# Optimization experiments

Measured on AMD Instinct MI355X. Metric: run time of the kernel, lower is better.

## Reference

```python
import jax, jax.numpy as jnp
import numpy as np

MARGIN_1 = 0.3
ALPHA_1 = 0.5
EPS = 1e-12
NEG = -1e30


def setup_inputs() -> dict:
    key = jax.random.key(0)
    batch_size = 128
    d = 2048
    N = 2 * batch_size
    feature = jax.random.normal(key, (N, d), dtype=jnp.float32)
    # PK-sampled ids: 32 identities x 4 instances, same ids in both modality halves
    num_ids = 32
    ids = jnp.repeat(jnp.arange(num_ids, dtype=jnp.int32), batch_size // num_ids)
    targets = jnp.concatenate([ids, ids])  # (N,)
    return {"feature": feature, "targets": targets}


def reference(feature, targets):
    N = feature.shape[0]
    # modality indicator: first half 0, second half 1 (self.sub)
    sub = jnp.arange(N) >= (N // 2)
    G = feature @ feature.T  # (N, N) gram matrix, symmetric

    pos_mat = targets[:, None] == targets[None, :]   # is_pos per anchor row
    intra_mat = sub[:, None] == sub[None, :]          # intra-modality per anchor row

    def msm(col_mask):
        # row-wise softmax of G restricted to columns in col_mask, zeros elsewhere
        logits = jnp.where(col_mask[None, :], G, NEG)
        return jax.nn.softmax(logits, axis=-1) * col_mask[None, :].astype(G.dtype)

    def trans(row_mask, col_mask):
        # ab: (intra rows -> cross cols) transition probs; ba: (cross -> intra)
        ab = msm(col_mask)
        ba = msm(row_mask)  # G symmetric, so softmax over row_mask cols == match.T softmax
        t = ab @ ba  # round-trip transition probability, valid on row_mask x row_mask
        return jnp.sqrt(jnp.clip(t, EPS))

    def masked_mean(v, m):
        mf = m.astype(v.dtype)
        w = mf[:, None] * mf[None, :]
        return jnp.sum(v * w) / jnp.sum(w)

    def per_anchor(is_pos, intra):
        is_neg = ~is_pos
        cross = ~intra
        mpi = is_pos & intra
        mpc = is_pos & cross
        mni = is_neg & intra
        mnc = is_neg & cross
        t_pos = trans(mpi, mpc)
        t_neg = trans(mni, mnc)
        loss_ap = masked_mean(jnp.clip(t_neg + (MARGIN_1 - ALPHA_1), 0.0, None), mni)
        loss_an = masked_mean(jnp.clip(ALPHA_1 - t_pos, 0.0, None), mpi)
        return loss_ap + loss_an

    loss = jnp.mean(jax.vmap(per_anchor)(pos_mat, intra_mat))

    # hard-mining accuracy over euclidean distance matrix
    sq = jnp.sum(feature * feature, axis=1)
    dist = jnp.sqrt(jnp.clip(sq[:, None] + sq[None, :] - 2.0 * G, EPS))
    dist_ap = jnp.max(jnp.where(pos_mat, dist, -jnp.inf), axis=1)
    dist_an = jnp.min(jnp.where(~pos_mat, dist, jnp.inf), axis=1)
    correct = jnp.sum((dist_an >= dist_ap).astype(jnp.int32))
    return loss, correct
```

## Files before the change

kernel.cpp:

```cpp
#include <hip/hip_runtime.h>

#define EPSF 1e-12f

typedef short bf16x8 __attribute__((ext_vector_type(8)));
typedef float f32x4 __attribute__((ext_vector_type(4)));

__device__ __forceinline__ unsigned short f2bf(float f) {
  unsigned int u = __float_as_uint(f);
  unsigned int r = u + 0x7fffu + ((u >> 16) & 1u);
  return (unsigned short)(r >> 16);
}

__global__ void gemm_tile(const float* __restrict__ F, float* __restrict__ Gout,
                          int n, int d, int kchunk) {
  __shared__ float As[64][36];
  __shared__ float Bs[64][36];
  const int tid = threadIdx.x;
  const int bx = blockIdx.x, by = blockIdx.y, kz = blockIdx.z;
  const int ty = tid >> 4, tx = tid & 15;
  const int lrow = tid >> 2;
  const int lcol = (tid & 3) * 8;
  const float* Ap = F + (size_t)(bx * 64 + lrow) * d + (size_t)kz * kchunk + lcol;
  const float* Bp = F + (size_t)(by * 64 + lrow) * d + (size_t)kz * kchunk + lcol;
  float acc[4][4];
  for (int r = 0; r < 4; r++)
    for (int c = 0; c < 4; c++) acc[r][c] = 0.0f;

  for (int ks = 0; ks < kchunk; ks += 32) {
    float4 a0 = *(const float4*)(Ap + ks);
    float4 a1 = *(const float4*)(Ap + ks + 4);
    float4 b0 = *(const float4*)(Bp + ks);
    float4 b1 = *(const float4*)(Bp + ks + 4);
    __syncthreads();
    *(float4*)&As[lrow][lcol]     = a0;
    *(float4*)&As[lrow][lcol + 4] = a1;
    *(float4*)&Bs[lrow][lcol]     = b0;
    *(float4*)&Bs[lrow][lcol + 4] = b1;
    __syncthreads();
#pragma unroll
    for (int kk = 0; kk < 32; kk += 4) {
      float4 av[4], bv[4];
#pragma unroll
      for (int r = 0; r < 4; r++) av[r] = *(const float4*)&As[ty + 16 * r][kk];
#pragma unroll
      for (int c = 0; c < 4; c++) bv[c] = *(const float4*)&Bs[tx + 16 * c][kk];
#pragma unroll
      for (int r = 0; r < 4; r++) {
        float4 A = av[r];
#pragma unroll
        for (int c = 0; c < 4; c++) {
          float4 B = bv[c];
          acc[r][c] += A.x * B.x + A.y * B.y + A.z * B.z + A.w * B.w;
        }
      }
    }
  }
  float* Gs = Gout + (size_t)kz * n * n;
#pragma unroll
  for (int r = 0; r < 4; r++)
#pragma unroll
    for (int c = 0; c < 4; c++)
      Gs[(size_t)(bx * 64 + ty + 16 * r) * n + (by * 64 + tx + 16 * c)] =
          acc[r][c];
}

__global__ void stats_kernel(const float* __restrict__ Gp,
                             const int* __restrict__ targets,
                             float* __restrict__ G, float* __restrict__ LSEtab,
                             float* __restrict__ flags, int n, int S) {
  __shared__ float bins[4][33];
  __shared__ int tg[256];
  __shared__ float diag[256];
  const int tid = threadIdx.x;
  const int lane = tid & 63;
  const int w = tid >> 6;
  const int nn = n * n;
  tg[tid] = targets[tid];
  {
    float s0 = 0.0f;
    for (int s = 0; s < S; s++)
      s0 += Gp[(size_t)s * nn + (size_t)tid * (n + 1)];
    diag[tid] = s0;
  }
  if (tid < 128) bins[tid >> 5][tid & 31] = 0.0f;
  __syncthreads();

  const int r = blockIdx.x * 4 + w;
  const int nhalf = n >> 1;
  const int opp0 = (r < nhalf) ? nhalf : 0;
  const int myid = tg[r];
  const float sqr = diag[r];

  float4 v = make_float4(0.f, 0.f, 0.f, 0.f);
  for (int s = 0; s < S; s++) {
    float4 t = *(const float4*)(Gp + (size_t)s * nn + (size_t)r * n + lane * 4);
    v.x += t.x; v.y += t.y; v.z += t.z; v.w += t.w;
  }
  *(float4*)(G + (size_t)r * n + lane * 4) = v;
  float gv[4] = {v.x, v.y, v.z, v.w};

  float dap = -1e30f, dan = 1e30f;
#pragma unroll
  for (int q = 0; q < 4; q++) {
    int j = lane * 4 + q;
    float dist = sqrtf(fmaxf(sqr + diag[j] - 2.0f * gv[q], EPSF));
    if (tg[j] == myid) dap = fmaxf(dap, dist);
    else               dan = fminf(dan, dist);
  }
#pragma unroll
  for (int off = 32; off; off >>= 1) {
    dap = fmaxf(dap, __shfl_xor(dap, off));
    dan = fminf(dan, __shfl_xor(dan, off));
  }
  if (lane == 0) flags[r] = (dan >= dap) ? 1.0f : 0.0f;

  float mx = -1e30f;
#pragma unroll
  for (int q = 0; q < 4; q++) {
    int j = lane * 4 + q;
    if (j >= opp0 && j < opp0 + nhalf) mx = fmaxf(mx, gv[q]);
  }
#pragma unroll
  for (int off = 32; off; off >>= 1) mx = fmaxf(mx, __shfl_xor(mx, off));

#pragma unroll
  for (int q = 0; q < 4; q++) {
    int j = lane * 4 + q;
    if (j >= opp0 && j < opp0 + nhalf)
      atomicAdd(&bins[w][tg[j]], __expf(gv[q] - mx));
  }
  __syncthreads();

  if (lane < 32) {
    float b = bins[w][lane];
    float lv = __shfl_up(b, 1, 32);
    if (lane == 0) lv = 0.0f;
#pragma unroll
    for (int off = 1; off < 32; off <<= 1) {
      float t = __shfl_up(lv, off, 32);
      if (lane >= off) lv += t;
    }
    float rv = __shfl_down(b, 1, 32);
    if (lane == 31) rv = 0.0f;
#pragma unroll
    for (int off = 1; off < 32; off <<= 1) {
      float t = __shfl_down(rv, off, 32);
      if (lane + off < 32) rv += t;
    }
    float excl = fmaxf(lv + rv, 1e-37f);
    LSEtab[(size_t)lane * n + r] = mx + __logf(excl);
  }
}

__global__ void TransitionLoss_30666066494151_kernel(
    const float* __restrict__ G, const int* __restrict__ targets,
    const float* __restrict__ LSEtab, float* __restrict__ lsp,
    float* __restrict__ lan, float* __restrict__ cnts, int n) {
  __shared__ unsigned short W[128][136];
  __shared__ int tg[256];
  __shared__ int maskA[128], maskB[128];
  __shared__ float Ri[128], Cl[128];
  __shared__ float SMRAW[16][17], SP[16][17], SQ[16][17];
  __shared__ float red[256];
  __shared__ int Plist[16], Qlist[16];
  __shared__ int ctrP, ctrQ;

  const int tid = threadIdx.x;
  const int cls = blockIdx.x;
  const int nhalf = n >> 1;
  const int myid = cls & 31;
  const int hA = cls >> 5;
  const int rowA0 = hA * nhalf;
  const int colB0 = nhalf - rowA0;

  tg[tid] = targets[tid];
  if (tid == 0) { ctrP = 0; ctrQ = 0; }
  __syncthreads();

  if (tid < 128) {
    maskA[tid] = (tg[rowA0 + tid] != myid) ? 1 : 0;
    Ri[tid] = LSEtab[(size_t)myid * n + rowA0 + tid];
  } else {
    maskB[tid - 128] = (tg[colB0 + tid - 128] != myid) ? 1 : 0;
    Cl[tid - 128] = LSEtab[(size_t)myid * n + colB0 + tid - 128];
  }
  if (tg[tid] == myid) {
    int inAhalf = (((tid >= nhalf) ? 1 : 0) == hA) ? 1 : 0;
    if (inAhalf) { int k = atomicAdd(&ctrP, 1); if (k < 16) Plist[k] = tid; }
    else         { int k = atomicAdd(&ctrQ, 1); if (k < 16) Qlist[k] = tid; }
  }
  __syncthreads();
  const int nP = min(ctrP, 16), nQ = min(ctrQ, 16);

#pragma unroll
  for (int k8 = 0; k8 < 2; k8++) {
    float4 g[8];
#pragma unroll
    for (int u = 0; u < 8; u++) {
      int e4 = tid + 256 * (k8 * 8 + u);
      int i = e4 >> 5;
      int l4 = (e4 & 31) << 2;
      g[u] = *(const float4*)(G + (size_t)(rowA0 + i) * n + colB0 + l4);
    }
#pragma unroll
    for (int u = 0; u < 8; u++) {
      int e4 = tid + 256 * (k8 * 8 + u);
      int i = e4 >> 5;
      int l4 = (e4 & 31) << 2;
      float rih = 0.5f * Ri[i];
      int ma = maskA[i];
      float w0 = (ma && maskB[l4 + 0]) ? __expf(g[u].x - rih - 0.5f * Cl[l4 + 0]) : 0.0f;
      float w1 = (ma && maskB[l4 + 1]) ? __expf(g[u].y - rih - 0.5f * Cl[l4 + 1]) : 0.0f;
      float w2 = (ma && maskB[l4 + 2]) ? __expf(g[u].z - rih - 0.5f * Cl[l4 + 2]) : 0.0f;
      float w3 = (ma && maskB[l4 + 3]) ? __expf(g[u].w - rih - 0.5f * Cl[l4 + 3]) : 0.0f;
      uint2 packed;
      packed.x = (unsigned)f2bf(w0) | ((unsigned)f2bf(w1) << 16);
      packed.y = (unsigned)f2bf(w2) | ((unsigned)f2bf(w3) << 16);
      *(uint2*)&W[i][l4] = packed;
    }
  }

  {
    int p = tid >> 4, q = tid & 15;
    float v = 0.0f;
    if (p < nP && q < nQ) v = G[(size_t)Plist[p] * n + Qlist[q]];
    SMRAW[p][q] = v;
  }
  __syncthreads();

  const int lane = tid & 63;
  const int wv = tid >> 6;
  const int m16 = lane & 15;
  const int kh = lane >> 4;
  f32x4 acc[2][8];
#pragma unroll
  for (int r = 0; r < 2; r++)
#pragma unroll
    for (int c = 0; c < 8; c++) acc[r][c] = (f32x4){0.f, 0.f, 0.f, 0.f};

#pragma unroll
  for (int kc = 0; kc < 4; kc++) {
    const int koff = kc * 32 + kh * 8;
    bf16x8 bfrag[8];
#pragma unroll
    for (int c = 0; c < 8; c++)
      bfrag[c] = *(const bf16x8*)&W[c * 16 + m16][koff];
#pragma unroll
    for (int r = 0; r < 2; r++) {
      bf16x8 afrag = bfrag[wv * 2 + r];
#pragma unroll
      for (int c = 0; c < 8; c++)
        acc[r][c] = __builtin_amdgcn_mfma_f32_16x16x32_bf16(
            afrag, bfrag[c], acc[r][c], 0, 0, 0);
    }
  }

  float lsum = 0.0f;
#pragma unroll
  for (int r = 0; r < 2; r++)
#pragma unroll
    for (int c = 0; c < 8; c++) {
      f32x4 D = acc[r][c];
      int jcol = c * 16 + m16;
      float rj = Ri[jcol];
#pragma unroll
      for (int e = 0; e < 4; e++) {
        int irow = wv * 32 + r * 16 + kh * 4 + e;
        float t = __expf(0.5f * (rj - Ri[irow])) * D[e];
        lsum += fmaxf(sqrtf(fmaxf(t, EPSF)) - 0.2f, 0.0f);
      }
    }
  red[tid] = lsum;
  __syncthreads();
  for (int s2 = 128; s2 > 0; s2 >>= 1) {
    if (tid < s2) red[tid] += red[tid + s2];
    __syncthreads();
  }
  if (tid == 0) lsp[cls] = red[0];

  __syncthreads();
  red[tid] = (tid < 128) ? (float)maskA[tid] : 0.0f;
  __syncthreads();
  for (int s2 = 128; s2 > 0; s2 >>= 1) {
    if (tid < s2) red[tid] += red[tid + s2];
    __syncthreads();
  }
  if (tid == 0) { cnts[cls * 2 + 0] = red[0]; cnts[cls * 2 + 1] = (float)nP; }

  if (tid < nP) {
    float mx = -1e30f;
    for (int q = 0; q < nQ; q++) mx = fmaxf(mx, SMRAW[tid][q]);
    float s = 0.0f;
    for (int q = 0; q < nQ; q++) s += __expf(SMRAW[tid][q] - mx);
    for (int q = 0; q < nQ; q++) SP[tid][q] = __expf(SMRAW[tid][q] - mx) / s;
  }
  if (tid >= 64 && tid < 64 + nQ) {
    int q = tid - 64;
    float mx = -1e30f;
    for (int p = 0; p < nP; p++) mx = fmaxf(mx, SMRAW[p][q]);
    float s = 0.0f;
    for (int p = 0; p < nP; p++) s += __expf(SMRAW[p][q] - mx);
    for (int p = 0; p < nP; p++) SQ[q][p] = __expf(SMRAW[p][q] - mx) / s;
  }
  __syncthreads();
  float lv = 0.0f;
  if (tid < nP * nP) {
    int i = tid / nP, j = tid - i * nP;
    float t = 0.0f;
    for (int l = 0; l < nQ; l++) t += SP[i][l] * SQ[l][j];
    lv = fmaxf(0.5f - sqrtf(fmaxf(t, EPSF)), 0.0f);
  }
  red[tid] = lv;
  __syncthreads();
  for (int s2 = 128; s2 > 0; s2 >>= 1) {
    if (tid < s2) red[tid] += red[tid + s2];
    __syncthreads();
  }
  if (tid == 0) lan[cls] = red[0];
}

__global__ void final_reduce(const float* __restrict__ lsp,
                             const float* __restrict__ lan,
                             const float* __restrict__ cnts,
                             const float* __restrict__ flags,
                             float* __restrict__ out, int n) {
  __shared__ float rl[256], rf[256];
  const int tid = threadIdx.x;
  float lv = 0.0f;
  if (tid < 64) {
    float nA = cnts[tid * 2 + 0];
    float nP = cnts[tid * 2 + 1];
    if (nP > 0.5f && nA > 0.5f)
      lv = nP * (lsp[tid] / (nA * nA) + lan[tid] / (nP * nP));
  }
  rl[tid] = lv;
  rf[tid] = flags[tid];
  __syncthreads();
  for (int s2 = 128; s2 > 0; s2 >>= 1) {
    if (tid < s2) { rl[tid] += rl[tid + s2]; rf[tid] += rf[tid + s2]; }
    __syncthreads();
  }
  if (tid == 0) {
    out[0] = rl[0] / (float)n;
    out[1] = rf[0];
  }
}

extern "C" void kernel_launch(void* const* d_in, const int* in_sizes, int n_in,
                              void* d_out, int out_size, void* d_ws,
                              size_t ws_size, hipStream_t stream) {
  const float* feature = (const float*)d_in[0];
  const int* targets = (const int*)d_in[1];
  const int n = in_sizes[1];
  const int d = in_sizes[0] / n;
  const int nn = n * n;
  const size_t small = 64 + 64 + 128 + 256 + (size_t)n * 32;

  int S = 1;
  if (ws_size >= (small + nn + (size_t)16 * nn) * sizeof(float)) S = 16;
  else if (ws_size >= (small + nn + (size_t)4 * nn) * sizeof(float)) S = 4;

  float* ws = (float*)d_ws;
  float* lsp = ws;
  float* lan = lsp + 64;
  float* cnts = lan + 64;
  float* flags = cnts + 128;
  float* LSEtab = flags + 256;
  float* G = LSEtab + (size_t)n * 32;
  float* Gp = (S > 1) ? (G + nn) : G;
  float* out = (float*)d_out;

  dim3 gg(n / 64, n / 64, S);
  gemm_tile<<<gg, 256, 0, stream>>>(feature, Gp, n, d, d / S);

  stats_kernel<<<n / 4, 256, 0, stream>>>(Gp, targets, G, LSEtab, flags, n, S);

  TransitionLoss_30666066494151_kernel<<<64, 256, 0, stream>>>(
      G, targets, LSEtab, lsp, lan, cnts, n);

  final_reduce<<<1, 256, 0, stream>>>(lsp, lan, cnts, flags, out, n);
}
```

Baseline: 62.37 us.

## Fuse four kernels into one persistent kernel with global atomic barriers

Merges the split-K GEMM, stats, transition-loss and final-reduce kernels into a single 256-block launch, replacing kernel boundaries with atomic-counter grid barriers and a shared-memory union. The aim is to remove launch gaps between the four stages. It adds a memset of the counters, spin-wait barriers that rely on all blocks being co-resident, and hardcodes the GEMM grid to 4x4 tiles with 256 blocks, which assumes S=16 and n=256.

```diff
diff --git a/kernel.cpp b/kernel.cpp
--- a/kernel.cpp
+++ b/kernel.cpp
@@ -11,338 +11,369 @@
   return (unsigned short)(r >> 16);
 }
 
-__global__ void gemm_tile(const float* __restrict__ F, float* __restrict__ Gout,
-                          int n, int d, int kchunk) {
-  __shared__ float As[64][36];
-  __shared__ float Bs[64][36];
+union SMem {
+  struct { float As[64][36]; float Bs[64][36]; } g;
+  struct {
+    unsigned short W[128][136];
+    int tg[256];
+    int maskA[128], maskB[128];
+    float Ri[128], Cl[128];
+    float SMRAW[16][17], SP[16][17], SQ[16][17];
+    float red[256];
+    int Plist[16], Qlist[16];
+    int ctrP, ctrQ;
+  } c;
+  struct { float bins[4][33]; int tg[256]; float diag[256]; } s;
+  struct { float rl[256]; float rf[256]; } f;
+};
+
+__device__ __forceinline__ void garrive(unsigned* ctr, int tid) {
+  __syncthreads();
+  if (tid == 0) {
+    __threadfence();
+    atomicAdd(ctr, 1u);
+  }
+}
+__device__ __forceinline__ void gbarrier(unsigned* ctr, unsigned tgt, int tid) {
+  __syncthreads();
+  if (tid == 0) {
+    __threadfence();
+    atomicAdd(ctr, 1u);
+    while (atomicAdd(ctr, 0u) < tgt) __builtin_amdgcn_s_sleep(1);
+    __threadfence();
+  }
+  __syncthreads();
+}
+
+__global__ __launch_bounds__(256, 2) void TransitionLoss_30666066494151_kernel(
+    const float* __restrict__ F, const int* __restrict__ targets,
+    unsigned* __restrict__ ctr, float* __restrict__ lsp,
+    float* __restrict__ lan, float* __restrict__ cnts,
+    float* __restrict__ flags, float* __restrict__ LSEtab,
+    float* __restrict__ G, float* __restrict__ Gp,
+    float* __restrict__ out, int n, int d, int S) {
+  __shared__ SMem sm;
   const int tid = threadIdx.x;
-  const int bx = blockIdx.x, by = blockIdx.y, kz = blockIdx.z;
-  const int ty = tid >> 4, tx = tid & 15;
-  const int lrow = tid >> 2;
-  const int lcol = (tid & 3) * 8;
-  const float* Ap = F + (size_t)(bx * 64 + lrow) * d + (size_t)kz * kchunk + lcol;
-  const float* Bp = F + (size_t)(by * 64 + lrow) * d + (size_t)kz * kchunk + lcol;
-  float acc[4][4];
-  for (int r = 0; r < 4; r++)
-    for (int c = 0; c < 4; c++) acc[r][c] = 0.0f;
-
-  for (int ks = 0; ks < kchunk; ks += 32) {
-    float4 a0 = *(const float4*)(Ap + ks);
-    float4 a1 = *(const float4*)(Ap + ks + 4);
-    float4 b0 = *(const float4*)(Bp + ks);
-    float4 b1 = *(const float4*)(Bp + ks + 4);
-    __syncthreads();
-    *(float4*)&As[lrow][lcol]     = a0;
-    *(float4*)&As[lrow][lcol + 4] = a1;
-    *(float4*)&Bs[lrow][lcol]     = b0;
-    *(float4*)&Bs[lrow][lcol + 4] = b1;
-    __syncthreads();
-#pragma unroll
-    for (int kk = 0; kk < 32; kk += 4) {
-      float4 av[4], bv[4];
-#pragma unroll
-      for (int r = 0; r < 4; r++) av[r] = *(const float4*)&As[ty + 16 * r][kk];
-#pragma unroll
-      for (int c = 0; c < 4; c++) bv[c] = *(const float4*)&Bs[tx + 16 * c][kk];
-#pragma unroll
-      for (int r = 0; r < 4; r++) {
-        float4 A = av[r];
-#pragma unroll
-        for (int c = 0; c < 4; c++) {
-          float4 B = bv[c];
-          acc[r][c] += A.x * B.x + A.y * B.y + A.z * B.z + A.w * B.w;
+  const int b = blockIdx.x;
+  const int nn = n * n;
+  const int nhalf = n >> 1;
+
+  if (b < 16 * S) {
+    const int bx = b & 3, by = (b >> 2) & 3, kz = b >> 4;
+    const int kchunk = d / S;
+    const int ty = tid >> 4, tx = tid & 15;
+    const int lrow = tid >> 2;
+    const int lcol = (tid & 3) * 8;
+    const float* Ap = F + (size_t)(bx * 64 + lrow) * d + (size_t)kz * kchunk + lcol;
+    const float* Bp = F + (size_t)(by * 64 + lrow) * d + (size_t)kz * kchunk + lcol;
+    float acc[4][4];
+    for (int r = 0; r < 4; r++)
+      for (int c = 0; c < 4; c++) acc[r][c] = 0.0f;
+
+    for (int ks = 0; ks < kchunk; ks += 32) {
+      float4 a0 = *(const float4*)(Ap + ks);
+      float4 a1 = *(const float4*)(Ap + ks + 4);
+      float4 b0 = *(const float4*)(Bp + ks);
+      float4 b1 = *(const float4*)(Bp + ks + 4);
+      __syncthreads();
+      *(float4*)&sm.g.As[lrow][lcol]     = a0;
+      *(float4*)&sm.g.As[lrow][lcol + 4] = a1;
+      *(float4*)&sm.g.Bs[lrow][lcol]     = b0;
+      *(float4*)&sm.g.Bs[lrow][lcol + 4] = b1;
+      __syncthreads();
+#pragma unroll
+      for (int kk = 0; kk < 32; kk += 4) {
+        float4 av[4], bv[4];
+#pragma unroll
+        for (int r = 0; r < 4; r++)
+          av[r] = *(const float4*)&sm.g.As[ty + 16 * r][kk];
+#pragma unroll
+        for (int c = 0; c < 4; c++)
+          bv[c] = *(const float4*)&sm.g.Bs[tx + 16 * c][kk];
+#pragma unroll
+        for (int r = 0; r < 4; r++) {
+          float4 A = av[r];
+#pragma unroll
+          for (int c = 0; c < 4; c++) {
+            float4 B = bv[c];
+            acc[r][c] += A.x * B.x + A.y * B.y + A.z * B.z + A.w * B.w;
+          }
         }
       }
     }
-  }
-  float* Gs = Gout + (size_t)kz * n * n;
-#pragma unroll
-  for (int r = 0; r < 4; r++)
-#pragma unroll
-    for (int c = 0; c < 4; c++)
-      Gs[(size_t)(bx * 64 + ty + 16 * r) * n + (by * 64 + tx + 16 * c)] =
-          acc[r][c];
-}
-
-__global__ void stats_kernel(const float* __restrict__ Gp,
-                             const int* __restrict__ targets,
-                             float* __restrict__ G, float* __restrict__ LSEtab,
-                             float* __restrict__ flags, int n, int S) {
-  __shared__ float bins[4][33];
-  __shared__ int tg[256];
-  __shared__ float diag[256];
-  const int tid = threadIdx.x;
-  const int lane = tid & 63;
-  const int w = tid >> 6;
-  const int nn = n * n;
-  tg[tid] = targets[tid];
+    float* Gs = Gp + (size_t)kz * nn;
+#pragma unroll
+    for (int r = 0; r < 4; r++)
+#pragma unroll
+      for (int c = 0; c < 4; c++)
+        Gs[(size_t)(bx * 64 + ty + 16 * r) * n + (by * 64 + tx + 16 * c)] =
+            acc[r][c];
+  }
+
+  if (b >= 64) { garrive(&ctr[0], tid); return; }
+  gbarrier(&ctr[0], 256, tid);
+
   {
-    float s0 = 0.0f;
-    for (int s = 0; s < S; s++)
-      s0 += Gp[(size_t)s * nn + (size_t)tid * (n + 1)];
-    diag[tid] = s0;
-  }
-  if (tid < 128) bins[tid >> 5][tid & 31] = 0.0f;
-  __syncthreads();
-
-  const int r = blockIdx.x * 4 + w;
-  const int nhalf = n >> 1;
-  const int opp0 = (r < nhalf) ? nhalf : 0;
-  const int myid = tg[r];
-  const float sqr = diag[r];
-
-  float4 v = make_float4(0.f, 0.f, 0.f, 0.f);
-  for (int s = 0; s < S; s++) {
-    float4 t = *(const float4*)(Gp + (size_t)s * nn + (size_t)r * n + lane * 4);
-    v.x += t.x; v.y += t.y; v.z += t.z; v.w += t.w;
-  }
-  *(float4*)(G + (size_t)r * n + lane * 4) = v;
-  float gv[4] = {v.x, v.y, v.z, v.w};
-
-  float dap = -1e30f, dan = 1e30f;
-#pragma unroll
-  for (int q = 0; q < 4; q++) {
-    int j = lane * 4 + q;
-    float dist = sqrtf(fmaxf(sqr + diag[j] - 2.0f * gv[q], EPSF));
-    if (tg[j] == myid) dap = fmaxf(dap, dist);
-    else               dan = fminf(dan, dist);
-  }
-#pragma unroll
-  for (int off = 32; off; off >>= 1) {
-    dap = fmaxf(dap, __shfl_xor(dap, off));
-    dan = fminf(dan, __shfl_xor(dan, off));
-  }
-  if (lane == 0) flags[r] = (dan >= dap) ? 1.0f : 0.0f;
-
-  float mx = -1e30f;
-#pragma unroll
-  for (int q = 0; q < 4; q++) {
-    int j = lane * 4 + q;
-    if (j >= opp0 && j < opp0 + nhalf) mx = fmaxf(mx, gv[q]);
-  }
-#pragma unroll
-  for (int off = 32; off; off >>= 1) mx = fmaxf(mx, __shfl_xor(mx, off));
-
-#pragma unroll
-  for (int q = 0; q < 4; q++) {
-    int j = lane * 4 + q;
-    if (j >= opp0 && j < opp0 + nhalf)
-      atomicAdd(&bins[w][tg[j]], __expf(gv[q] - mx));
-  }
-  __syncthreads();
-
-  if (lane < 32) {
-    float b = bins[w][lane];
-    float lv = __shfl_up(b, 1, 32);
-    if (lane == 0) lv = 0.0f;
-#pragma unroll
-    for (int off = 1; off < 32; off <<= 1) {
-      float t = __shfl_up(lv, off, 32);
-      if (lane >= off) lv += t;
-    }
-    float rv = __shfl_down(b, 1, 32);
-    if (lane == 31) rv = 0.0f;
-#pragma unroll
-    for (int off = 1; off < 32; off <<= 1) {
-      float t = __shfl_down(rv, off, 32);
-      if (lane + off < 32) rv += t;
-    }
-    float excl = fmaxf(lv + rv, 1e-37f);
-    LSEtab[(size_t)lane * n + r] = mx + __logf(excl);
-  }
-}
-
-__global__ void TransitionLoss_30666066494151_kernel(
-    const float* __restrict__ G, const int* __restrict__ targets,
-    const float* __restrict__ LSEtab, float* __restrict__ lsp,
-    float* __restrict__ lan, float* __restrict__ cnts, int n) {
-  __shared__ unsigned short W[128][136];
-  __shared__ int tg[256];
-  __shared__ int maskA[128], maskB[128];
-  __shared__ float Ri[128], Cl[128];
-  __shared__ float SMRAW[16][17], SP[16][17], SQ[16][17];
-  __shared__ float red[256];
-  __shared__ int Plist[16], Qlist[16];
-  __shared__ int ctrP, ctrQ;
-
-  const int tid = threadIdx.x;
-  const int cls = blockIdx.x;
-  const int nhalf = n >> 1;
-  const int myid = cls & 31;
-  const int hA = cls >> 5;
-  const int rowA0 = hA * nhalf;
-  const int colB0 = nhalf - rowA0;
-
-  tg[tid] = targets[tid];
-  if (tid == 0) { ctrP = 0; ctrQ = 0; }
-  __syncthreads();
-
-  if (tid < 128) {
-    maskA[tid] = (tg[rowA0 + tid] != myid) ? 1 : 0;
-    Ri[tid] = LSEtab[(size_t)myid * n + rowA0 + tid];
-  } else {
-    maskB[tid - 128] = (tg[colB0 + tid - 128] != myid) ? 1 : 0;
-    Cl[tid - 128] = LSEtab[(size_t)myid * n + colB0 + tid - 128];
-  }
-  if (tg[tid] == myid) {
-    int inAhalf = (((tid >= nhalf) ? 1 : 0) == hA) ? 1 : 0;
-    if (inAhalf) { int k = atomicAdd(&ctrP, 1); if (k < 16) Plist[k] = tid; }
-    else         { int k = atomicAdd(&ctrQ, 1); if (k < 16) Qlist[k] = tid; }
-  }
-  __syncthreads();
-  const int nP = min(ctrP, 16), nQ = min(ctrQ, 16);
-
-#pragma unroll
-  for (int k8 = 0; k8 < 2; k8++) {
-    float4 g[8];
-#pragma unroll
-    for (int u = 0; u < 8; u++) {
-      int e4 = tid + 256 * (k8 * 8 + u);
-      int i = e4 >> 5;
-      int l4 = (e4 & 31) << 2;
-      g[u] = *(const float4*)(G + (size_t)(rowA0 + i) * n + colB0 + l4);
-    }
-#pragma unroll
-    for (int u = 0; u < 8; u++) {
-      int e4 = tid + 256 * (k8 * 8 + u);
-      int i = e4 >> 5;
-      int l4 = (e4 & 31) << 2;
-      float rih = 0.5f * Ri[i];
-      int ma = maskA[i];
-      float w0 = (ma && maskB[l4 + 0]) ? __expf(g[u].x - rih - 0.5f * Cl[l4 + 0]) : 0.0f;
-      float w1 = (ma && maskB[l4 + 1]) ? __expf(g[u].y - rih - 0.5f * Cl[l4 + 1]) : 0.0f;
-      float w2 = (ma && maskB[l4 + 2]) ? __expf(g[u].z - rih - 0.5f * Cl[l4 + 2]) : 0.0f;
-      float w3 = (ma && maskB[l4 + 3]) ? __expf(g[u].w - rih - 0.5f * Cl[l4 + 3]) : 0.0f;
-      uint2 packed;
-      packed.x = (unsigned)f2bf(w0) | ((unsigned)f2bf(w1) << 16);
-      packed.y = (unsigned)f2bf(w2) | ((unsigned)f2bf(w3) << 16);
-      *(uint2*)&W[i][l4] = packed;
-    }
-  }
+    const int lane = tid & 63;
+    const int w = tid >> 6;
+    sm.s.tg[tid] = targets[tid];
+    {
+      float s0 = 0.0f;
+      for (int s = 0; s < S; s++)
+        s0 += Gp[(size_t)s * nn + (size_t)tid * (n + 1)];
+      sm.s.diag[tid] = s0;
+    }
+    if (tid < 128) sm.s.bins[tid >> 5][tid & 31] = 0.0f;
+    __syncthreads();
+
+    const int r = b * 4 + w;
+    const int opp0 = (r < nhalf) ? nhalf : 0;
+    const int myid = sm.s.tg[r];
+    const float sqr = sm.s.diag[r];
+
+    float4 v = make_float4(0.f, 0.f, 0.f, 0.f);
+    for (int s = 0; s < S; s++) {
+      float4 t = *(const float4*)(Gp + (size_t)s * nn + (size_t)r * n + lane * 4);
+      v.x += t.x; v.y += t.y; v.z += t.z; v.w += t.w;
+    }
+    *(float4*)(G + (size_t)r * n + lane * 4) = v;
+    float gv[4] = {v.x, v.y, v.z, v.w};
+
+    float dap = -1e30f, dan = 1e30f;
+#pragma unroll
+    for (int q = 0; q < 4; q++) {
+      int j = lane * 4 + q;
+      float dist = sqrtf(fmaxf(sqr + sm.s.diag[j] - 2.0f * gv[q], EPSF));
+      if (sm.s.tg[j] == myid) dap = fmaxf(dap, dist);
+      else                    dan = fminf(dan, dist);
+    }
+#pragma unroll
+    for (int off = 32; off; off >>= 1) {
+      dap = fmaxf(dap, __shfl_xor(dap, off));
+      dan = fminf(dan, __shfl_xor(dan, off));
+    }
+    if (lane == 0) flags[r] = (dan >= dap) ? 1.0f : 0.0f;
+
+    float mx = -1e30f;
+#pragma unroll
+    for (int q = 0; q < 4; q++) {
+      int j = lane * 4 + q;
+      if (j >= opp0 && j < opp0 + nhalf) mx = fmaxf(mx, gv[q]);
+    }
+#pragma unroll
+    for (int off = 32; off; off >>= 1) mx = fmaxf(mx, __shfl_xor(mx, off));
+
+#pragma unroll
+    for (int q = 0; q < 4; q++) {
+      int j = lane * 4 + q;
+      if (j >= opp0 && j < opp0 + nhalf)
+        atomicAdd(&sm.s.bins[w][sm.s.tg[j]], __expf(gv[q] - mx));
+    }
+    __syncthreads();
+
+    if (lane < 32) {
+      float bb = sm.s.bins[w][lane];
+      float lv = __shfl_up(bb, 1, 32);
+      if (lane == 0) lv = 0.0f;
+#pragma unroll
+      for (int off = 1; off < 32; off <<= 1) {
+        float t = __shfl_up(lv, off, 32);
+        if (lane >= off) lv += t;
+      }
+      float rvv = __shfl_down(bb, 1, 32);
+      if (lane == 31) rvv = 0.0f;
+#pragma unroll
+      for (int off = 1; off < 32; off <<= 1) {
+        float t = __shfl_down(rvv, off, 32);
+        if (lane + off < 32) rvv += t;
+      }
+      float excl = fmaxf(lv + rvv, 1e-37f);
+      LSEtab[(size_t)lane * n + r] = mx + __logf(excl);
+    }
+  }
+
+  gbarrier(&ctr[1], 64, tid);
 
   {
-    int p = tid >> 4, q = tid & 15;
-    float v = 0.0f;
-    if (p < nP && q < nQ) v = G[(size_t)Plist[p] * n + Qlist[q]];
-    SMRAW[p][q] = v;
-  }
-  __syncthreads();
-
-  const int lane = tid & 63;
-  const int wv = tid >> 6;
-  const int m16 = lane & 15;
-  const int kh = lane >> 4;
-  f32x4 acc[2][8];
-#pragma unroll
-  for (int r = 0; r < 2; r++)
-#pragma unroll
-    for (int c = 0; c < 8; c++) acc[r][c] = (f32x4){0.f, 0.f, 0.f, 0.f};
-
-#pragma unroll
-  for (int kc = 0; kc < 4; kc++) {
-    const int koff = kc * 32 + kh * 8;
-    bf16x8 bfrag[8];
-#pragma unroll
-    for (int c = 0; c < 8; c++)
-      bfrag[c] = *(const bf16x8*)&W[c * 16 + m16][koff];
-#pragma unroll
-    for (int r = 0; r < 2; r++) {
-      bf16x8 afrag = bfrag[wv * 2 + r];
+    const int cls = b;
+    const int myid = cls & 31;
+    const int hA = cls >> 5;
+    const int rowA0 = hA * nhalf;
+    const int colB0 = nhalf - rowA0;
+
+    sm.c.tg[tid] = targets[tid];
+    if (tid == 0) { sm.c.ctrP = 0; sm.c.ctrQ = 0; }
+    __syncthreads();
+
+    if (tid < 128) {
+      sm.c.maskA[tid] = (sm.c.tg[rowA0 + tid] != myid) ? 1 : 0;
+      sm.c.Ri[tid] = LSEtab[(size_t)myid * n + rowA0 + tid];
+    } else {
+      sm.c.maskB[tid - 128] = (sm.c.tg[colB0 + tid - 128] != myid) ? 1 : 0;
+      sm.c.Cl[tid - 128] = LSEtab[(size_t)myid * n + colB0 + tid - 128];
+    }
+    if (sm.c.tg[tid] == myid) {
+      int inAhalf = (((tid >= nhalf) ? 1 : 0) == hA) ? 1 : 0;
+      if (inAhalf) { int k = atomicAdd(&sm.c.ctrP, 1); if (k < 16) sm.c.Plist[k] = tid; }
+      else         { int k = atomicAdd(&sm.c.ctrQ, 1); if (k < 16) sm.c.Qlist[k] = tid; }
+    }
+    __syncthreads();
+    const int nP = min(sm.c.ctrP, 16), nQ = min(sm.c.ctrQ, 16);
+
+#pragma unroll
+    for (int k8 = 0; k8 < 2; k8++) {
+      float4 g[8];
+#pragma unroll
+      for (int u = 0; u < 8; u++) {
+        int e4 = tid + 256 * (k8 * 8 + u);
+        int i = e4 >> 5;
+        int l4 = (e4 & 31) << 2;
+        g[u] = *(const float4*)(G + (size_t)(rowA0 + i) * n + colB0 + l4);
+      }
+#pragma unroll
+      for (int u = 0; u < 8; u++) {
+        int e4 = tid + 256 * (k8 * 8 + u);
+        int i = e4 >> 5;
+        int l4 = (e4 & 31) << 2;
+        float rih = 0.5f * sm.c.Ri[i];
+        int ma = sm.c.maskA[i];
+        float w0 = (ma && sm.c.maskB[l4 + 0]) ? __expf(g[u].x - rih - 0.5f * sm.c.Cl[l4 + 0]) : 0.0f;
+        float w1 = (ma && sm.c.maskB[l4 + 1]) ? __expf(g[u].y - rih - 0.5f * sm.c.Cl[l4 + 1]) : 0.0f;
+        float w2 = (ma && sm.c.maskB[l4 + 2]) ? __expf(g[u].z - rih - 0.5f * sm.c.Cl[l4 + 2]) : 0.0f;
+        float w3 = (ma && sm.c.maskB[l4 + 3]) ? __expf(g[u].w - rih - 0.5f * sm.c.Cl[l4 + 3]) : 0.0f;
+        uint2 packed;
+        packed.x = (unsigned)f2bf(w0) | ((unsigned)f2bf(w1) << 16);
+        packed.y = (unsigned)f2bf(w2) | ((unsigned)f2bf(w3) << 16);
+        *(uint2*)&sm.c.W[i][l4] = packed;
+      }
+    }
+
+    {
+      int p = tid >> 4, q = tid & 15;
+      float v = 0.0f;
+      if (p < nP && q < nQ) v = G[(size_t)sm.c.Plist[p] * n + sm.c.Qlist[q]];
+      sm.c.SMRAW[p][q] = v;
+    }
+    __syncthreads();
+
+    const int lane = tid & 63;
+    const int wv = tid >> 6;
+    const int m16 = lane & 15;
+    const int kh = lane >> 4;
+    f32x4 acc[2][8];
+#pragma unroll
+    for (int r = 0; r < 2; r++)
+#pragma unroll
+      for (int c = 0; c < 8; c++) acc[r][c] = (f32x4){0.f, 0.f, 0.f, 0.f};
+
+#pragma unroll
+    for (int kc = 0; kc < 4; kc++) {
+      const int koff = kc * 32 + kh * 8;
+      bf16x8 bfrag[8];
 #pragma unroll
       for (int c = 0; c < 8; c++)
-        acc[r][c] = __builtin_amdgcn_mfma_f32_16x16x32_bf16(
-            afrag, bfrag[c], acc[r][c], 0, 0, 0);
-    }
-  }
-
-  float lsum = 0.0f;
-#pragma unroll
-  for (int r = 0; r < 2; r++)
-#pragma unroll
-    for (int c = 0; c < 8; c++) {
-      f32x4 D = acc[r][c];
-      int jcol = c * 16 + m16;
-      float rj = Ri[jcol];
-#pragma unroll
-      for (int e = 0; e < 4; e++) {
-        int irow = wv * 32 + r * 16 + kh * 4 + e;
-        float t = __expf(0.5f * (rj - Ri[irow])) * D[e];
-        lsum += fmaxf(sqrtf(fmaxf(t, EPSF)) - 0.2f, 0.0f);
-      }
-    }
-  red[tid] = lsum;
-  __syncthreads();
-  for (int s2 = 128; s2 > 0; s2 >>= 1) {
-    if (tid < s2) red[tid] += red[tid + s2];
-    __syncthreads();
-  }
-  if (tid == 0) lsp[cls] = red[0];
-
-  __syncthreads();
-  red[tid] = (tid < 128) ? (float)maskA[tid] : 0.0f;
-  __syncthreads();
-  for (int s2 = 128; s2 > 0; s2 >>= 1) {
-    if (tid < s2) red[tid] += red[tid + s2];
-    __syncthreads();
-  }
-  if (tid == 0) { cnts[cls * 2 + 0] = red[0]; cnts[cls * 2 + 1] = (float)nP; }
-
-  if (tid < nP) {
-    float mx = -1e30f;
-    for (int q = 0; q < nQ; q++) mx = fmaxf(mx, SMRAW[tid][q]);
-    float s = 0.0f;
-    for (int q = 0; q < nQ; q++) s += __expf(SMRAW[tid][q] - mx);
-    for (int q = 0; q < nQ; q++) SP[tid][q] = __expf(SMRAW[tid][q] - mx) / s;
-  }
-  if (tid >= 64 && tid < 64 + nQ) {
-    int q = tid - 64;
-    float mx = -1e30f;
-    for (int p = 0; p < nP; p++) mx = fmaxf(mx, SMRAW[p][q]);
-    float s = 0.0f;
-    for (int p = 0; p < nP; p++) s += __expf(SMRAW[p][q] - mx);
-    for (int p = 0; p < nP; p++) SQ[q][p] = __expf(SMRAW[p][q] - mx) / s;
-  }
-  __syncthreads();
-  float lv = 0.0f;
-  if (tid < nP * nP) {
-    int i = tid / nP, j = tid - i * nP;
-    float t = 0.0f;
-    for (int l = 0; l < nQ; l++) t += SP[i][l] * SQ[l][j];
-    lv = fmaxf(0.5f - sqrtf(fmaxf(t, EPSF)), 0.0f);
-  }
-  red[tid] = lv;
-  __syncthreads();
-  for (int s2 = 128; s2 > 0; s2 >>= 1) {
-    if (tid < s2) red[tid] += red[tid + s2];
-    __syncthreads();
-  }
-  if (tid == 0) lan[cls] = red[0];
-}
-
-__global__ void final_reduce(const float* __restrict__ lsp,
-                             const float* __restrict__ lan,
-                             const float* __restrict__ cnts,
-                             const float* __restrict__ flags,
-                             float* __restrict__ out, int n) {
-  __shared__ float rl[256], rf[256];
-  const int tid = threadIdx.x;
-  float lv = 0.0f;
-  if (tid < 64) {
-    float nA = cnts[tid * 2 + 0];
-    float nP = cnts[tid * 2 + 1];
-    if (nP > 0.5f && nA > 0.5f)
-      lv = nP * (lsp[tid] / (nA * nA) + lan[tid] / (nP * nP));
-  }
-  rl[tid] = lv;
-  rf[tid] = flags[tid];
-  __syncthreads();
-  for (int s2 = 128; s2 > 0; s2 >>= 1) {
-    if (tid < s2) { rl[tid] += rl[tid + s2]; rf[tid] += rf[tid + s2]; }
-    __syncthreads();
-  }
-  if (tid == 0) {
-    out[0] = rl[0] / (float)n;
-    out[1] = rf[0];
+        bfrag[c] = *(const bf16x8*)&sm.c.W[c * 16 + m16][koff];
+#pragma unroll
+      for (int r = 0; r < 2; r++) {
+        bf16x8 afrag = bfrag[wv * 2 + r];
+#pragma unroll
+        for (int c = 0; c < 8; c++)
+          acc[r][c] = __builtin_amdgcn_mfma_f32_16x16x32_bf16(
+              afrag, bfrag[c], acc[r][c], 0, 0, 0);
+      }
+    }
+
+    float lsum = 0.0f;
+#pragma unroll
+    for (int r = 0; r < 2; r++)
+#pragma unroll
+      for (int c = 0; c < 8; c++) {
+        f32x4 D = acc[r][c];
+        int jcol = c * 16 + m16;
+        float rj = sm.c.Ri[jcol];
+#pragma unroll
+        for (int e = 0; e < 4; e++) {
+          int irow = wv * 32 + r * 16 + kh * 4 + e;
+          float t = __expf(0.5f * (rj - sm.c.Ri[irow])) * D[e];
+          lsum += fmaxf(sqrtf(fmaxf(t, EPSF)) - 0.2f, 0.0f);
+        }
+      }
+    sm.c.red[tid] = lsum;
+    __syncthreads();
+    for (int s2 = 128; s2 > 0; s2 >>= 1) {
+      if (tid < s2) sm.c.red[tid] += sm.c.red[tid + s2];
+      __syncthreads();
+    }
+    if (tid == 0) lsp[cls] = sm.c.red[0];
+
+    __syncthreads();
+    sm.c.red[tid] = (tid < 128) ? (float)sm.c.maskA[tid] : 0.0f;
+    __syncthreads();
+    for (int s2 = 128; s2 > 0; s2 >>= 1) {
+      if (tid < s2) sm.c.red[tid] += sm.c.red[tid + s2];
+      __syncthreads();
+    }
+    if (tid == 0) { cnts[cls * 2 + 0] = sm.c.red[0]; cnts[cls * 2 + 1] = (float)nP; }
+
+    if (tid < nP) {
+      float mx = -1e30f;
+      for (int q = 0; q < nQ; q++) mx = fmaxf(mx, sm.c.SMRAW[tid][q]);
+      float s = 0.0f;
+      for (int q = 0; q < nQ; q++) s += __expf(sm.c.SMRAW[tid][q] - mx);
+      for (int q = 0; q < nQ; q++)
+        sm.c.SP[tid][q] = __expf(sm.c.SMRAW[tid][q] - mx) / s;
+    }
+    if (tid >= 64 && tid < 64 + nQ) {
+      int q = tid - 64;
+      float mx = -1e30f;
+      for (int p = 0; p < nP; p++) mx = fmaxf(mx, sm.c.SMRAW[p][q]);
+      float s = 0.0f;
+      for (int p = 0; p < nP; p++) s += __expf(sm.c.SMRAW[p][q] - mx);
+      for (int p = 0; p < nP; p++)
+        sm.c.SQ[q][p] = __expf(sm.c.SMRAW[p][q] - mx) / s;
+    }
+    __syncthreads();
+    float lv = 0.0f;
+    if (tid < nP * nP) {
+      int i = tid / nP, j = tid - i * nP;
+      float t = 0.0f;
+      for (int l = 0; l < nQ; l++) t += sm.c.SP[i][l] * sm.c.SQ[l][j];
+      lv = fmaxf(0.5f - sqrtf(fmaxf(t, EPSF)), 0.0f);
+    }
+    sm.c.red[tid] = lv;
+    __syncthreads();
+    for (int s2 = 128; s2 > 0; s2 >>= 1) {
+      if (tid < s2) sm.c.red[tid] += sm.c.red[tid + s2];
+      __syncthreads();
+    }
+    if (tid == 0) lan[cls] = sm.c.red[0];
+  }
+
+  if (b != 0) { garrive(&ctr[2], tid); return; }
+  gbarrier(&ctr[2], 64, tid);
+
+  {
+    float lv = 0.0f;
+    if (tid < 64) {
+      float nA = cnts[tid * 2 + 0];
+      float nP = cnts[tid * 2 + 1];
+      if (nP > 0.5f && nA > 0.5f)
+        lv = nP * (lsp[tid] / (nA * nA) + lan[tid] / (nP * nP));
+    }
+    sm.f.rl[tid] = lv;
+    sm.f.rf[tid] = flags[tid];
+    __syncthreads();
+    for (int s2 = 128; s2 > 0; s2 >>= 1) {
+      if (tid < s2) {
+        sm.f.rl[tid] += sm.f.rl[tid + s2];
+        sm.f.rf[tid] += sm.f.rf[tid + s2];
+      }
+      __syncthreads();
+    }
+    if (tid == 0) {
+      out[0] = sm.f.rl[0] / (float)n;
+      out[1] = sm.f.rf[0];
+    }
   }
 }
 
@@ -354,14 +385,15 @@
   const int n = in_sizes[1];
   const int d = in_sizes[0] / n;
   const int nn = n * n;
-  const size_t small = 64 + 64 + 128 + 256 + (size_t)n * 32;
+  const size_t smallf = 16 + 64 + 64 + 128 + 256 + (size_t)n * 32;
 
   int S = 1;
-  if (ws_size >= (small + nn + (size_t)16 * nn) * sizeof(float)) S = 16;
-  else if (ws_size >= (small + nn + (size_t)4 * nn) * sizeof(float)) S = 4;
-
-  float* ws = (float*)d_ws;
-  float* lsp = ws;
+  if (ws_size >= (smallf + nn + (size_t)16 * nn) * sizeof(float)) S = 16;
+  else if (ws_size >= (smallf + nn + (size_t)4 * nn) * sizeof(float)) S = 4;
+
+  unsigned* ctr = (unsigned*)d_ws;
+  float* base = (float*)d_ws + 16;
+  float* lsp = base;
   float* lan = lsp + 64;
   float* cnts = lan + 64;
   float* flags = cnts + 128;
@@ -370,13 +402,8 @@
   float* Gp = (S > 1) ? (G + nn) : G;
   float* out = (float*)d_out;
 
-  dim3 gg(n / 64, n / 64, S);
-  gemm_tile<<<gg, 256, 0, stream>>>(feature, Gp, n, d, d / S);
-
-  stats_kernel<<<n / 4, 256, 0, stream>>>(Gp, targets, G, LSEtab, flags, n, S);
-
-  TransitionLoss_30666066494151_kernel<<<64, 256, 0, stream>>>(
-      G, targets, LSEtab, lsp, lan, cnts, n);
-
-  final_reduce<<<1, 256, 0, stream>>>(lsp, lan, cnts, flags, out, n);
+  hipMemsetAsync(d_ws, 0, 16 * sizeof(unsigned), stream);
+
+  TransitionLoss_30666066494151_kernel<<<256, 256, 0, stream>>>(
+      feature, targets, ctr, lsp, lan, cnts, flags, LSEtab, G, Gp, out, n, d, S);
 }
```

Result: slower. 180.6 us (+189.6%).
